# Optimization experiments

Hardware: AMD Instinct MI355X
Metric: run time of the kernel (lower is better)

## Reference

```python
import jax, jax.numpy as jnp
import numpy as np

N_NODES = 4_194_304
N_GRAPHS = 65_536

# Orthonormal (Frobenius) basis for symmetric traceless 3x3 matrices: the
# real l=2 components of 1o x 1o -> 2e (Clebsch-Gordan up to basis choice).
_s2 = 1.0 / np.sqrt(2.0)
_B = np.zeros((5, 3, 3), dtype=np.float32)
_B[0, 0, 1] = _B[0, 1, 0] = _s2            # xy
_B[1, 1, 2] = _B[1, 2, 1] = _s2            # yz
_B[2, 0, 2] = _B[2, 2, 0] = _s2            # xz
_B[3, 0, 0] = _s2; _B[3, 1, 1] = -_s2      # x^2 - y^2
_B[4, 0, 0] = _B[4, 1, 1] = -1.0 / np.sqrt(6.0); _B[4, 2, 2] = 2.0 / np.sqrt(6.0)
B_CG = jnp.asarray(_B)

INV_SQRT2 = 0.7071067811865476
INV_SQRT3 = 0.5773502691896258


def setup_inputs() -> dict:
    key = jax.random.key(0)
    k1, k2, k3, k4, k5, k6 = jax.random.split(key, 6)
    z = jax.random.randint(k1, (N_NODES,), 0, 100, dtype=jnp.int32)
    pos = jax.random.normal(k2, (N_NODES, 3), dtype=jnp.float32)
    batch = jnp.sort(jax.random.randint(k3, (N_NODES,), 0, N_GRAPHS, dtype=jnp.int32))
    # FullyConnectedTensorProduct weights: 5 paths, mul pattern (1,1,mul_out)
    # 0e*0e->2x0e (2) + 1o*1o->2x0e (2) + 0e*1o->2x1o (2) + 1o*0e->2x1o (2) + 1o*1o->1x2e (1) = 9
    w_tp = jax.random.normal(k4, (9,), dtype=jnp.float32)
    fc_w = jax.random.normal(k5, (1, 13), dtype=jnp.float32) / np.sqrt(13.0)
    fc_b = jax.random.normal(k6, (1,), dtype=jnp.float32) * 0.01
    return {"z": z, "pos": pos, "batch": batch, "w_tp": w_tp, "fc_w": fc_w, "fc_b": fc_b}


def reference(z, pos, batch, w_tp, fc_w, fc_b):
    s = z.astype(jnp.float32)                      # [N] scalar (0e) part
    v = pos                                        # [N,3] vector (1o) part
    wA, wB = w_tp[0:2], w_tp[2:4]                  # -> 2x0e paths
    wC, wD = w_tp[4:6], w_tp[6:8]                  # -> 2x1o paths
    wE = w_tp[8]                                   # -> 1x2e path

    # CG tensor product x (x) x -> 2x0e + 2x1o + 1x2e, path-normalized by 1/sqrt(#paths)
    ss = s * s                                     # 0e x 0e -> 0e
    dot = jnp.sum(v * v, axis=-1)                  # 1o . 1o -> 0e (CG = delta/sqrt3)
    out0 = (ss[:, None] * wA + (dot * INV_SQRT3)[:, None] * wB) * INV_SQRT2   # [N,2]
    sv = s[:, None] * v                            # 0e x 1o -> 1o
    out1 = (sv[:, None, :] * (wC + wD)[None, :, None]) * INV_SQRT2            # [N,2,3]
    quad = jnp.einsum('kij,ni,nj->nk', B_CG, v, v) # 1o x 1o -> 2e            # [N,5]
    out2 = wE * quad

    x = jnp.concatenate([out0, out1.reshape(-1, 6), out2], axis=-1)  # [N,13]
    x = jax.nn.relu(x)                             # (as in source: relu on all irreps)
    y = x @ fc_w.T + fc_b                          # [N,1] -> 1x0e
    y = jnp.tanh(y)                                # Gate on pure scalars = scalar act

    sums = jax.ops.segment_sum(y, batch, num_segments=N_GRAPHS)                # [G,1]
    counts = jax.ops.segment_sum(jnp.ones((batch.shape[0], 1), y.dtype), batch,
                                 num_segments=N_GRAPHS)
    return sums / jnp.maximum(counts, 1.0)
```

## Files before the change

kernel.cpp:

```cpp
#include <hip/hip_runtime.h>

static constexpr float INV_SQRT2 = 0.70710678118654752f;
static constexpr float INV_SQRT3 = 0.57735026918962576f;
static constexpr float SQRT2     = 1.41421356237309505f;
static constexpr float INV_SQRT6 = 0.40824829046386302f;

static constexpr int W_GRAPHS = 8;

__device__ __forceinline__ float fast_tanh(float x) {
    const float e = __builtin_amdgcn_exp2f(x * 2.8853900817779268f);
    const float r = __builtin_amdgcn_rcpf(e + 1.0f);
    return fmaf(-2.0f, r, 1.0f);
}

__device__ __forceinline__ float gate_p(float k, float fw) { return k > 0.f ? k * fw : 0.f; }
__device__ __forceinline__ float gate_n(float k, float fw) { return k < 0.f ? k * fw : 0.f; }

__global__ __launch_bounds__(256) void e3nn_fused(
    const int*   __restrict__ z,
    const float* __restrict__ pos,
    const int*   __restrict__ batch,
    const float* __restrict__ w_tp,
    const float* __restrict__ fc_w,
    const float* __restrict__ fc_b,
    float*       __restrict__ out,
    int n, int n_graphs)
{
    const int lane = threadIdx.x & 63;
    const int wave = (blockIdx.x * blockDim.x + threadIdx.x) >> 6;
    const int g0   = wave * W_GRAPHS;
    if (g0 >= n_graphs) return;

    const float kA0 = w_tp[0] * INV_SQRT2;
    const float kA1 = w_tp[1] * INV_SQRT2;
    const float kB0 = w_tp[2] * (INV_SQRT3 * INV_SQRT2);
    const float kB1 = w_tp[3] * (INV_SQRT3 * INV_SQRT2);
    const float c0  = (w_tp[4] + w_tp[6]) * INV_SQRT2;
    const float c1  = (w_tp[5] + w_tp[7]) * INV_SQRT2;
    const float wE  = w_tp[8];
    const float fw0 = fc_w[0], fw1 = fc_w[1];
    const float fb  = fc_b[0];

    const float P0 = gate_p(c0, fc_w[2]) + gate_p(c1, fc_w[5]);
    const float N0 = gate_n(c0, fc_w[2]) + gate_n(c1, fc_w[5]);
    const float P1 = gate_p(c0, fc_w[3]) + gate_p(c1, fc_w[6]);
    const float N1 = gate_n(c0, fc_w[3]) + gate_n(c1, fc_w[6]);
    const float P2 = gate_p(c0, fc_w[4]) + gate_p(c1, fc_w[7]);
    const float N2 = gate_n(c0, fc_w[4]) + gate_n(c1, fc_w[7]);
    const float k8  = wE * SQRT2,     k11 = wE * INV_SQRT2, k12 = wE * INV_SQRT6;
    const float P8  = gate_p(k8,  fc_w[8]),  N8  = gate_n(k8,  fc_w[8]);
    const float P9  = gate_p(k8,  fc_w[9]),  N9  = gate_n(k8,  fc_w[9]);
    const float P10 = gate_p(k8,  fc_w[10]), N10 = gate_n(k8,  fc_w[10]);
    const float P11 = gate_p(k11, fc_w[11]), N11 = gate_n(k11, fc_w[11]);
    const float P12 = gate_p(k12, fc_w[12]), N12 = gate_n(k12, fc_w[12]);

    const int tl     = (lane < W_GRAPHS) ? lane : W_GRAPHS;
    const int target = g0 + tl;
    unsigned p2 = 1;
    while (p2 < (unsigned)n) p2 <<= 1;
    int bval = 0;
    for (unsigned step = p2 >> 1; step > 0; step >>= 1) {
        const unsigned cand = (unsigned)bval + step;
        if (cand <= (unsigned)n && batch[cand - 1] < target) bval = (int)cand;
    }

    const int nb = __shfl_down(bval, 1);
    const int B0 = __shfl(bval, 0), B1 = __shfl(bval, 1);
    const int B2 = __shfl(bval, 2), B3 = __shfl(bval, 3);
    const int B4 = __shfl(bval, 4), B5 = __shfl(bval, 5);
    const int B6 = __shfl(bval, 6), B7 = __shfl(bval, 7);
    const int B8 = __shfl(bval, 8);

    float a0 = 0.f, a1 = 0.f, a2 = 0.f, a3 = 0.f;
    float a4 = 0.f, a5 = 0.f, a6 = 0.f, a7 = 0.f;

#pragma unroll 1
    for (int base = B0; base < B8; base += 64) {
        const int i = base + lane;
        if (i < B8) {
            const float sc = (float)z[i];
            const float v0 = pos[i * 3 + 0];
            const float v1 = pos[i * 3 + 1];
            const float v2 = pos[i * 3 + 2];

            const float v00 = v0 * v0, v11 = v1 * v1, v22 = v2 * v2;
            const float ss  = sc * sc;
            const float dr  = v00 + v11 + v22;

            float acc = fb;
            const float x0 = fmaf(ss, kA0, dr * kB0);
            const float x1 = fmaf(ss, kA1, dr * kB1);
            acc = fmaf(fmaxf(x0, 0.f), fw0, acc);
            acc = fmaf(fmaxf(x1, 0.f), fw1, acc);

            const float sv0 = sc * v0, sv1 = sc * v1, sv2 = sc * v2;
            acc = fmaf(sv0, (sv0 > 0.f ? P0 : N0), acc);
            acc = fmaf(sv1, (sv1 > 0.f ? P1 : N1), acc);
            acc = fmaf(sv2, (sv2 > 0.f ? P2 : N2), acc);

            const float t8 = v0 * v1, t9 = v1 * v2, t10 = v0 * v2;
            acc = fmaf(t8,  (t8  > 0.f ? P8  : N8 ), acc);
            acc = fmaf(t9,  (t9  > 0.f ? P9  : N9 ), acc);
            acc = fmaf(t10, (t10 > 0.f ? P10 : N10), acc);

            const float t11 = v00 - v11;
            acc = fmaf(t11, (t11 > 0.f ? P11 : N11), acc);
            const float t12 = (v22 - v00) + (v22 - v11);
            acc = fmaf(t12, (t12 > 0.f ? P12 : N12), acc);

            const float y = fast_tanh(acc);

            const bool ge1 = i >= B1, ge2 = i >= B2, ge3 = i >= B3;
            const bool ge4 = i >= B4, ge5 = i >= B5, ge6 = i >= B6;
            const bool ge7 = i >= B7;
            a0 += (!ge1)        ? y : 0.f;
            a1 += (ge1 && !ge2) ? y : 0.f;
            a2 += (ge2 && !ge3) ? y : 0.f;
            a3 += (ge3 && !ge4) ? y : 0.f;
            a4 += (ge4 && !ge5) ? y : 0.f;
            a5 += (ge5 && !ge6) ? y : 0.f;
            a6 += (ge6 && !ge7) ? y : 0.f;
            a7 += (ge7)         ? y : 0.f;
        }
    }

#pragma unroll
    for (int off = 32; off >= 1; off >>= 1) {
        a0 += __shfl_xor(a0, off);
        a1 += __shfl_xor(a1, off);
        a2 += __shfl_xor(a2, off);
        a3 += __shfl_xor(a3, off);
        a4 += __shfl_xor(a4, off);
        a5 += __shfl_xor(a5, off);
        a6 += __shfl_xor(a6, off);
        a7 += __shfl_xor(a7, off);
    }

    if (lane < W_GRAPHS && g0 + lane < n_graphs) {
        float sel = (lane == 0) ? a0
                  : (lane == 1) ? a1
                  : (lane == 2) ? a2
                  : (lane == 3) ? a3
                  : (lane == 4) ? a4
                  : (lane == 5) ? a5
                  : (lane == 6) ? a6
                  :               a7;
        const float c = (float)(nb - bval);
        out[g0 + lane] = sel / fmaxf(c, 1.0f);
    }
}

extern "C" void kernel_launch(void* const* d_in, const int* in_sizes, int n_in,
                              void* d_out, int out_size, void* d_ws, size_t ws_size,
                              hipStream_t stream) {
    const int*   z     = (const int*)d_in[0];
    const float* pos   = (const float*)d_in[1];
    const int*   batch = (const int*)d_in[2];
    const float* w_tp  = (const float*)d_in[3];
    const float* fc_w  = (const float*)d_in[4];
    const float* fc_b  = (const float*)d_in[5];

    float* out = (float*)d_out;
    const int n        = in_sizes[0];
    const int n_graphs = out_size;

    const int waves = (n_graphs + W_GRAPHS - 1) / W_GRAPHS;
    const int blocks = (waves * 64 + 255) / 256;
    e3nn_fused<<<blocks, 256, 0, stream>>>(z, pos, batch, w_tp, fc_w, fc_b,
                                           out, n, n_graphs);
}
```

Before: 27.61 us.

## Seed segment search locally, process two nodes per lane with register prefetch

Replaces the full-range binary search for graph boundaries with a local search over a 64K window around the expected position (target*64), falling back to the full search if any lane's result fails verification. The main loop now handles two consecutive nodes per lane using int2 and paired float3 loads, and software-prefetches the next 128-node chunk into registers. A launch-bounds occupancy hint is added. The aims are fewer dependent global loads in the search and more memory-level parallelism in the streaming loop. The costs are extra verification loads, higher register pressure, and a seed that depends on the average nodes per graph.

```diff
diff --git a/kernel.cpp b/kernel.cpp
--- a/kernel.cpp
+++ b/kernel.cpp
@@ -16,7 +16,9 @@
 __device__ __forceinline__ float gate_p(float k, float fw) { return k > 0.f ? k * fw : 0.f; }
 __device__ __forceinline__ float gate_n(float k, float fw) { return k < 0.f ? k * fw : 0.f; }
 
-__global__ __launch_bounds__(256) void e3nn_fused(
+struct F3 { float x, y, zc; };
+
+__global__ __launch_bounds__(256, 6) void e3nn_fused(
     const int*   __restrict__ z,
     const float* __restrict__ pos,
     const int*   __restrict__ batch,
@@ -56,12 +58,26 @@
 
     const int tl     = (lane < W_GRAPHS) ? lane : W_GRAPHS;
     const int target = g0 + tl;
-    unsigned p2 = 1;
-    while (p2 < (unsigned)n) p2 <<= 1;
-    int bval = 0;
-    for (unsigned step = p2 >> 1; step > 0; step >>= 1) {
-        const unsigned cand = (unsigned)bval + step;
-        if (cand <= (unsigned)n && batch[cand - 1] < target) bval = (int)cand;
+    long long seed = (long long)target * 64 - 32768;
+    int lo = seed < 0 ? 0 : (seed > n ? n : (int)seed);
+    int bval = lo;
+    #pragma unroll 1
+    for (int step = 32768; step > 0; step >>= 1) {
+        const int cand = bval + step;
+        if (cand <= n && batch[cand - 1] < target) bval = cand;
+    }
+    {
+        const bool ok = (bval == 0 || batch[bval - 1] < target) &&
+                        (bval >= n || batch[bval] >= target);
+        if (!__all(ok)) {
+            unsigned p2 = 1;
+            while (p2 < (unsigned)n) p2 <<= 1;
+            bval = 0;
+            for (unsigned step = p2; step > 0; step >>= 1) {
+                const unsigned cand = (unsigned)bval + step;
+                if (cand <= (unsigned)n && batch[cand - 1] < target) bval = (int)cand;
+            }
+        }
     }
 
     const int nb = __shfl_down(bval, 1);
@@ -74,53 +90,77 @@
     float a0 = 0.f, a1 = 0.f, a2 = 0.f, a3 = 0.f;
     float a4 = 0.f, a5 = 0.f, a6 = 0.f, a7 = 0.f;
 
-#pragma unroll 1
-    for (int base = B0; base < B8; base += 64) {
-        const int i = base + lane;
-        if (i < B8) {
-            const float sc = (float)z[i];
-            const float v0 = pos[i * 3 + 0];
-            const float v1 = pos[i * 3 + 1];
-            const float v2 = pos[i * 3 + 2];
-
-            const float v00 = v0 * v0, v11 = v1 * v1, v22 = v2 * v2;
-            const float ss  = sc * sc;
-            const float dr  = v00 + v11 + v22;
-
-            float acc = fb;
-            const float x0 = fmaf(ss, kA0, dr * kB0);
-            const float x1 = fmaf(ss, kA1, dr * kB1);
-            acc = fmaf(fmaxf(x0, 0.f), fw0, acc);
-            acc = fmaf(fmaxf(x1, 0.f), fw1, acc);
-
-            const float sv0 = sc * v0, sv1 = sc * v1, sv2 = sc * v2;
-            acc = fmaf(sv0, (sv0 > 0.f ? P0 : N0), acc);
-            acc = fmaf(sv1, (sv1 > 0.f ? P1 : N1), acc);
-            acc = fmaf(sv2, (sv2 > 0.f ? P2 : N2), acc);
-
-            const float t8 = v0 * v1, t9 = v1 * v2, t10 = v0 * v2;
-            acc = fmaf(t8,  (t8  > 0.f ? P8  : N8 ), acc);
-            acc = fmaf(t9,  (t9  > 0.f ? P9  : N9 ), acc);
-            acc = fmaf(t10, (t10 > 0.f ? P10 : N10), acc);
-
-            const float t11 = v00 - v11;
-            acc = fmaf(t11, (t11 > 0.f ? P11 : N11), acc);
-            const float t12 = (v22 - v00) + (v22 - v11);
-            acc = fmaf(t12, (t12 > 0.f ? P12 : N12), acc);
-
-            const float y = fast_tanh(acc);
-
-            const bool ge1 = i >= B1, ge2 = i >= B2, ge3 = i >= B3;
-            const bool ge4 = i >= B4, ge5 = i >= B5, ge6 = i >= B6;
-            const bool ge7 = i >= B7;
-            a0 += (!ge1)        ? y : 0.f;
-            a1 += (ge1 && !ge2) ? y : 0.f;
-            a2 += (ge2 && !ge3) ? y : 0.f;
-            a3 += (ge3 && !ge4) ? y : 0.f;
-            a4 += (ge4 && !ge5) ? y : 0.f;
-            a5 += (ge5 && !ge6) ? y : 0.f;
-            a6 += (ge6 && !ge7) ? y : 0.f;
-            a7 += (ge7)         ? y : 0.f;
+    auto body = [&](int i, float sc, float v0, float v1, float v2) {
+        const float v00 = v0 * v0, v11 = v1 * v1, v22 = v2 * v2;
+        const float ss  = sc * sc;
+        const float dr  = v00 + v11 + v22;
+
+        float acc = fb;
+        const float x0 = fmaf(ss, kA0, dr * kB0);
+        const float x1 = fmaf(ss, kA1, dr * kB1);
+        acc = fmaf(fmaxf(x0, 0.f), fw0, acc);
+        acc = fmaf(fmaxf(x1, 0.f), fw1, acc);
+
+        const float sv0 = sc * v0, sv1 = sc * v1, sv2 = sc * v2;
+        acc = fmaf(sv0, (sv0 > 0.f ? P0 : N0), acc);
+        acc = fmaf(sv1, (sv1 > 0.f ? P1 : N1), acc);
+        acc = fmaf(sv2, (sv2 > 0.f ? P2 : N2), acc);
+
+        const float t8 = v0 * v1, t9 = v1 * v2, t10 = v0 * v2;
+        acc = fmaf(t8,  (t8  > 0.f ? P8  : N8 ), acc);
+        acc = fmaf(t9,  (t9  > 0.f ? P9  : N9 ), acc);
+        acc = fmaf(t10, (t10 > 0.f ? P10 : N10), acc);
+
+        const float t11 = v00 - v11;
+        acc = fmaf(t11, (t11 > 0.f ? P11 : N11), acc);
+        const float t12 = (v22 - v00) + (v22 - v11);
+        acc = fmaf(t12, (t12 > 0.f ? P12 : N12), acc);
+
+        float y = fast_tanh(acc);
+        y = ((unsigned)(i - B0) < (unsigned)(B8 - B0)) ? y : 0.f;
+
+        const bool ge1 = i >= B1, ge2 = i >= B2, ge3 = i >= B3;
+        const bool ge4 = i >= B4, ge5 = i >= B5, ge6 = i >= B6;
+        const bool ge7 = i >= B7;
+        a0 += (!ge1)        ? y : 0.f;
+        a1 += (ge1 && !ge2) ? y : 0.f;
+        a2 += (ge2 && !ge3) ? y : 0.f;
+        a3 += (ge3 && !ge4) ? y : 0.f;
+        a4 += (ge4 && !ge5) ? y : 0.f;
+        a5 += (ge5 && !ge6) ? y : 0.f;
+        a6 += (ge6 && !ge7) ? y : 0.f;
+        a7 += (ge7)         ? y : 0.f;
+    };
+
+    if (B0 < B8) {
+        const int first = B0 & ~1;
+        const int lastEven = (B8 - 1) & ~1;
+
+        auto pidx = [&](int ii) {
+            int c = ii < lastEven ? ii : lastEven;
+            return c < 0 ? 0 : c;
+        };
+
+        int ic = pidx(first + 2 * lane);
+        int2 zz = *reinterpret_cast<const int2*>(z + ic);
+        F3  pa  = *reinterpret_cast<const F3*>(pos + 3 * ic);
+        F3  pb  = *reinterpret_cast<const F3*>(pos + 3 * ic + 3);
+
+        #pragma unroll 1
+        for (int base = first; base < B8; base += 128) {
+            int2 zzn = {0, 0};
+            F3 pan = {0.f, 0.f, 0.f}, pbn = {0.f, 0.f, 0.f};
+            const bool more = (base + 128) < B8;
+            if (more) {
+                const int jc = pidx(base + 128 + 2 * lane);
+                zzn = *reinterpret_cast<const int2*>(z + jc);
+                pan = *reinterpret_cast<const F3*>(pos + 3 * jc);
+                pbn = *reinterpret_cast<const F3*>(pos + 3 * jc + 3);
+            }
+            const int i0 = base + 2 * lane;
+            body(i0,     (float)zz.x, pa.x, pa.y, pa.zc);
+            body(i0 + 1, (float)zz.y, pb.x, pb.y, pb.zc);
+            zz = zzn; pa = pan; pb = pbn;
         }
     }
 
@@ -164,7 +204,7 @@
     const int n        = in_sizes[0];
     const int n_graphs = out_size;
 
-    const int waves = (n_graphs + W_GRAPHS - 1) / W_GRAPHS;
+    const int waves  = (n_graphs + W_GRAPHS - 1) / W_GRAPHS;
     const int blocks = (waves * 64 + 255) / 256;
     e3nn_fused<<<blocks, 256, 0, stream>>>(z, pos, batch, w_tp, fc_w, fc_b,
                                            out, n, n_graphs);
```

After: 31.60 us. 1.14x slower.
